# Kernel tuning notes

Hardware: AMD Instinct MI355X
Metric: run time of the kernel (lower is better)

The kernel has to match this reference:

```python
import jax, jax.numpy as jnp
import numpy as np

N_NODES = 100000
NEG_SLOPE = 0.2


def gat_conv(x, edge_index, W, a_src, a_dst, bias):
    """PyG GATConv, heads=1, concat, add_self_loops=True."""
    N = x.shape[0]
    loop = jnp.arange(N, dtype=edge_index.dtype)
    src = jnp.concatenate([edge_index[0], loop])  # message sources j
    dst = jnp.concatenate([edge_index[1], loop])  # message targets i
    h = x @ W                                      # [N, out]
    asrc = h @ a_src                               # [N]
    adst = h @ a_dst                               # [N]
    e = jax.nn.leaky_relu(asrc[src] + adst[dst], NEG_SLOPE)   # [E+N]
    m = jax.ops.segment_max(e, dst, num_segments=N)           # per-dst max
    w = jnp.exp(e - jax.lax.stop_gradient(m)[dst])
    denom = jax.ops.segment_sum(w, dst, num_segments=N)
    alpha = w / denom[dst]                                     # softmax per dst
    out = jax.ops.segment_sum(alpha[:, None] * h[src], dst, num_segments=N)
    return out + bias


def setup_inputs() -> dict:
    key = jax.random.key(0)
    ks = jax.random.split(key, 16)
    N, E, D = N_NODES, 3200000, 128
    x = jax.random.normal(ks[0], (N, D), dtype=jnp.float32)
    edge_index = jax.random.randint(ks[1], (2, E), 0, N, dtype=jnp.int64)
    def glorot(k, shape):
        fan = sum(shape)
        return jax.random.uniform(k, shape, jnp.float32, -1.0, 1.0) * np.sqrt(6.0 / fan)
    return {
        "x": x,
        "edge_index": edge_index,
        "W1": glorot(ks[2], (D, 16)),
        "a1_src": glorot(ks[3], (16,)),
        "a1_dst": glorot(ks[4], (16,)),
        "b1": jnp.zeros((16,), jnp.float32),
        "W2": glorot(ks[5], (16, 10)),
        "a2_src": glorot(ks[6], (10,)),
        "a2_dst": glorot(ks[7], (10,)),
        "b2": jnp.zeros((10,), jnp.float32),
        "Wl1": glorot(ks[8], (10, 10)),
        "bl1": jnp.zeros((10,), jnp.float32),
        "Wl2": glorot(ks[9], (10, 1)),
        "bl2": jnp.zeros((1,), jnp.float32),
    }


def reference(x, edge_index, W1, a1_src, a1_dst, b1, W2, a2_src, a2_dst, b2,
              Wl1, bl1, Wl2, bl2):
    h = gat_conv(x, edge_index, W1, a1_src, a1_dst, b1)
    h = jax.nn.relu(h)
    h = gat_conv(h, edge_index, W2, a2_src, a2_dst, b2)
    h = h @ Wl1 + bl1
    h = jax.nn.relu(h)
    return h @ Wl2 + bl2  # [N, 1]
```

## Files before the change

kernel.cpp:

```cpp
#include <hip/hip_runtime.h>
#include <hip/hip_fp16.h>


#define NEG 0.2f
#define FSH 7
#define BNODES 128
#define NSBMAX 1024
#define CAPB 4608
#define TILE 4096
#define EPT 8
#define PES 9
#define LOFSTR 132

__device__ __forceinline__ float lrelu(float x) { return x > 0.0f ? x : NEG * x; }

__device__ __forceinline__ unsigned fenc(float f) {
    unsigned u = __float_as_uint(f);
    return (u & 0x80000000u) ? ~u : (u | 0x80000000u);
}
__device__ __forceinline__ float fdec(unsigned e) {
    return (e & 0x80000000u) ? __uint_as_float(e & 0x7FFFFFFFu) : __uint_as_float(~e);
}

__device__ __forceinline__ float4 ldh4(const __half* h, size_t off) {
    uint2 u = *(const uint2*)(h + off);
    __half2 a = *(__half2*)&u.x, b = *(__half2*)&u.y;
    float2 fa = __half22float2(a), fb = __half22float2(b);
    return make_float4(fa.x, fa.y, fb.x, fb.y);
}

__global__ __launch_bounds__(512) void k_front(
    const float* __restrict__ x, const float* __restrict__ W1,
    const float* __restrict__ a1s, const float* __restrict__ a1d,
    __half* __restrict__ h1, float* __restrict__ s1, float* __restrict__ d1,
    unsigned* __restrict__ gmax,
    const int* __restrict__ esrc, const int* __restrict__ edst,
    int* __restrict__ bcur, unsigned* __restrict__ pairs,
    int N, int E, int NG, int NC, int NSB)
{
    __shared__ float smem[9224];
    int tid = threadIdx.x;
    int bid = blockIdx.x;
    long long T = (long long)NG + NC;
    int before = (int)(((long long)bid * NC) / T);
    int isc = (int)((((long long)bid + 1) * NC) / T) > before;

    if (isc) {
        unsigned* lsrt = (unsigned*)smem;
        int* lhist = (int*)smem + TILE;
        int* lofs  = lhist + NSBMAX;
        int* gbase = lofs + NSBMAX;
        int* wsum  = gbase + NSBMAX;
        unsigned short* rid = (unsigned short*)(smem + TILE + 3 * NSBMAX + 8);
        int cid = before;
        int base = cid * TILE;
        int tcnt = min(TILE, E - base);
        for (int i = tid; i < NSB; i += 512) lhist[i] = 0;
        __syncthreads();
        int ed[EPT];
#pragma unroll
        for (int u = 0; u < EPT; ++u) {
            int i = tid + u * 512;
            ed[u] = (i < tcnt) ? edst[base + i] : -1;
            if (ed[u] >= 0) atomicAdd(&lhist[ed[u] >> FSH], 1);
        }
        __syncthreads();
        int i0 = 2 * tid;
        int a = (i0 < NSB) ? lhist[i0] : 0;
        int b = (i0 + 1 < NSB) ? lhist[i0 + 1] : 0;
        int s = a + b, pfx = s;
#pragma unroll
        for (int off = 1; off < 64; off <<= 1) {
            int t = __shfl_up(pfx, off, 64);
            if ((tid & 63) >= off) pfx += t;
        }
        if ((tid & 63) == 63) wsum[tid >> 6] = pfx;
        __syncthreads();
        int carry = 0;
        for (int w = 0; w < (tid >> 6); ++w) carry += wsum[w];
        int excl = pfx + carry - s;
        if (i0 < NSB) {
            lofs[i0] = excl;
            gbase[i0] = a ? atomicAdd(&bcur[i0 * 16], a) : 0;
        }
        if (i0 + 1 < NSB) {
            lofs[i0 + 1] = excl + a;
            gbase[i0 + 1] = b ? atomicAdd(&bcur[(i0 + 1) * 16], b) : 0;
        }
        __syncthreads();
        if (i0 < NSB) lhist[i0] = lofs[i0];
        if (i0 + 1 < NSB) lhist[i0 + 1] = lofs[i0 + 1];
        __syncthreads();
#pragma unroll
        for (int u = 0; u < EPT; ++u) {
            int i = tid + u * 512;
            if (ed[u] >= 0) {
                int d = ed[u], srcv = esrc[base + i];
                int bb = d >> FSH;
                int pos = atomicAdd(&lhist[bb], 1);
                lsrt[pos] = ((unsigned)(d & (BNODES - 1)) << 17) | (unsigned)srcv;
                rid[pos] = (unsigned short)bb;
            }
        }
        __syncthreads();
#pragma unroll
        for (int u = 0; u < EPT; ++u) {
            int i = tid + u * 512;
            if (i < tcnt) {
                int r = rid[i];
                int rel = gbase[r] + (i - lofs[r]);
                if (rel < CAPB) pairs[(size_t)r * CAPB + rel] = lsrt[i];
            }
        }
        return;
    }

    float* sW = smem;
    float* wm = smem + 2060;
    int gid = bid - before;
    for (int i = tid; i < 2048; i += 512) sW[i + ((i >> 9) << 2)] = W1[i];
    int node0 = gid * 128;
    int node = node0 + (tid >> 2);
    int q = tid & 3;
    bool valid = node < N;
    float4 xr[8];
    {
        const float4* xp = (const float4*)x + (size_t)node * 32 + q * 8;
#pragma unroll
        for (int k = 0; k < 8; ++k)
            xr[k] = valid ? xp[k] : make_float4(0.f, 0.f, 0.f, 0.f);
    }
    __syncthreads();

    float acc[16];
#pragma unroll
    for (int c = 0; c < 16; ++c) acc[c] = 0.f;
    int wbase = q * 516;
#pragma unroll
    for (int k = 0; k < 8; ++k) {
        float xs0 = xr[k].x, xs1 = xr[k].y, xs2 = xr[k].z, xs3 = xr[k].w;
#pragma unroll
        for (int t = 0; t < 4; ++t) {
            float xv = (t == 0) ? xs0 : (t == 1) ? xs1 : (t == 2) ? xs2 : xs3;
            const float4* wrow = (const float4*)&sW[wbase + (k * 4 + t) * 16];
            float4 w0 = wrow[0], w1 = wrow[1], w2 = wrow[2], w3 = wrow[3];
            acc[0]  += xv * w0.x; acc[1]  += xv * w0.y; acc[2]  += xv * w0.z; acc[3]  += xv * w0.w;
            acc[4]  += xv * w1.x; acc[5]  += xv * w1.y; acc[6]  += xv * w1.z; acc[7]  += xv * w1.w;
            acc[8]  += xv * w2.x; acc[9]  += xv * w2.y; acc[10] += xv * w2.z; acc[11] += xv * w2.w;
            acc[12] += xv * w3.x; acc[13] += xv * w3.y; acc[14] += xv * w3.z; acc[15] += xv * w3.w;
        }
    }
#pragma unroll
    for (int c = 0; c < 16; ++c) {
        acc[c] += __shfl_xor(acc[c], 1);
        acc[c] += __shfl_xor(acc[c], 2);
    }
    float sv = 0.f, dv = 0.f;
    {
        const float4* asp = (const float4*)a1s;
        const float4* adp = (const float4*)a1d;
#pragma unroll
        for (int r = 0; r < 4; ++r) {
            float4 as = asp[r], ad = adp[r];
            sv += acc[r*4+0]*as.x + acc[r*4+1]*as.y + acc[r*4+2]*as.z + acc[r*4+3]*as.w;
            dv += acc[r*4+0]*ad.x + acc[r*4+1]*ad.y + acc[r*4+2]*ad.z + acc[r*4+3]*ad.w;
        }
    }
    if (valid) {
        float4 av;
        if      (q == 0) av = make_float4(acc[0],  acc[1],  acc[2],  acc[3]);
        else if (q == 1) av = make_float4(acc[4],  acc[5],  acc[6],  acc[7]);
        else if (q == 2) av = make_float4(acc[8],  acc[9],  acc[10], acc[11]);
        else             av = make_float4(acc[12], acc[13], acc[14], acc[15]);
        __half2 p0 = __floats2half2_rn(av.x, av.y);
        __half2 p1 = __floats2half2_rn(av.z, av.w);
        uint2 u; u.x = *(unsigned*)&p0; u.y = *(unsigned*)&p1;
        *(uint2*)&h1[(size_t)node * 16 + q * 4] = u;
        if (q == 0) { s1[node] = sv; d1[node] = dv; }
    }
    float m = valid ? sv : -3.4e38f;
#pragma unroll
    for (int off = 32; off >= 1; off >>= 1) m = fmaxf(m, __shfl_xor(m, off));
    if ((tid & 63) == 0) wm[tid >> 6] = m;
    __syncthreads();
    if (tid == 0) {
        float bmx = wm[0];
#pragma unroll
        for (int i = 1; i < 8; ++i) bmx = fmaxf(bmx, wm[i]);
        atomicMax(gmax, fenc(bmx));
    }
}

__global__ __launch_bounds__(512) void k_agg1(
    const int* __restrict__ bcur, unsigned* __restrict__ pairs,
    const int* __restrict__ esrc, const int* __restrict__ edst,
    const float* __restrict__ s1, const float* __restrict__ d1, const __half* __restrict__ h1,
    const float* __restrict__ b1, const float* __restrict__ W2,
    const float* __restrict__ a2s, const float* __restrict__ a2d,
    __half* __restrict__ h2, float* __restrict__ s2, float* __restrict__ d2,
    const unsigned* __restrict__ gmax1p, unsigned* __restrict__ gmax2,
    int* __restrict__ lofs_g, int N, int E)
{
    __shared__ unsigned srt[CAPB];
    __shared__ float accs[BNODES * 17];
    __shared__ int lcnt[BNODES];
    __shared__ int lofs[BNODES + 1];
    __shared__ float dds[BNODES], mbs[BNODES];
    __shared__ float sW[160], sb[16], sas[16], sad[16];
    __shared__ int wsum[8];
    __shared__ float wm[8];

    int tid = threadIdx.x;
    int fb = blockIdx.x;
    if (tid < 160) sW[tid] = W2[tid];
    if (tid < 16) {
        sb[tid]  = b1[tid];
        sas[tid] = (tid < 10) ? a2s[tid] : 0.f;
        sad[tid] = (tid < 10) ? a2d[tid] : 0.f;
    }
    int node0 = fb << FSH;
    float g0 = fdec(*gmax1p);
    if (tid < BNODES) {
        int n = node0 + tid;
        float dd = (n < N) ? d1[n] : 0.f;
        dds[tid] = dd; mbs[tid] = lrelu(g0 + dd);
        lcnt[tid] = 0;
    }
    __syncthreads();

    int rbase = fb * CAPB;
    int cnt = bcur[fb * 16];
    int gg = tid >> 2, q = tid & 3;

    if (cnt <= CAPB) {
        unsigned pe[PES];
#pragma unroll
        for (int u = 0; u < PES; ++u) {
            int i = tid + u * 512;
            bool ok = (i < cnt);
            pe[u] = ok ? pairs[rbase + i] : 0u;
            if (ok) atomicAdd(&lcnt[(pe[u] >> 17) & (BNODES - 1)], 1);
        }
        __syncthreads();
        int c = (tid < BNODES) ? lcnt[tid] : 0;
        int pfx = c;
#pragma unroll
        for (int off = 1; off < 64; off <<= 1) {
            int t = __shfl_up(pfx, off, 64);
            if ((tid & 63) >= off) pfx += t;
        }
        if ((tid & 63) == 63) wsum[tid >> 6] = pfx;
        __syncthreads();
        int carry = 0;
        for (int w = 0; w < (tid >> 6); ++w) carry += wsum[w];
        pfx += carry;
        if (tid < BNODES) { lofs[tid + 1] = pfx; lcnt[tid] = pfx - c; }
        if (tid == 0) lofs[0] = 0;
        __syncthreads();
#pragma unroll
        for (int u = 0; u < PES; ++u) {
            int i = tid + u * 512;
            if (i < cnt) {
                unsigned p = pe[u];
                int pos = atomicAdd(&lcnt[(p >> 17) & (BNODES - 1)], 1);
                srt[pos] = p & 0x1FFFF;
            }
        }
        __syncthreads();

#pragma unroll
        for (int u = 0; u < PES; ++u) {
            int i = tid + u * 512;
            if (i < cnt) pairs[rbase + i] = srt[i];
        }
        if (tid <= BNODES) lofs_g[fb * LOFSTR + tid] = lofs[tid];
        if (tid == 0) lofs_g[fb * LOFSTR + BNODES + 1] = 1;

        int n = node0 + gg;
        float4 accv; float den;
        if (n < N) {
            float w = __expf(lrelu(s1[n] + dds[gg]) - mbs[gg]);
            float4 hv = ldh4(h1, (size_t)n * 16 + 4 * q);
            accv = make_float4(w * hv.x, w * hv.y, w * hv.z, w * hv.w);
            den = w;
        } else { accv = make_float4(0.f, 0.f, 0.f, 0.f); den = 0.f; }
        {
            float dd = dds[gg], mb = mbs[gg];
            int j = lofs[gg], j1 = lofs[gg + 1];
            for (; j + 4 <= j1; j += 4) {
                int e0 = srt[j], e1 = srt[j + 1], e2 = srt[j + 2], e3 = srt[j + 3];
                float4 H0 = ldh4(h1, (size_t)e0 * 16 + 4 * q);
                float4 H1 = ldh4(h1, (size_t)e1 * 16 + 4 * q);
                float4 H2 = ldh4(h1, (size_t)e2 * 16 + 4 * q);
                float4 H3 = ldh4(h1, (size_t)e3 * 16 + 4 * q);
                int eq = srt[j + q];
                float wq = __expf(lrelu(s1[eq] + dd) - mb);
                float w0 = __shfl(wq, 0, 4), w1 = __shfl(wq, 1, 4);
                float w2 = __shfl(wq, 2, 4), w3 = __shfl(wq, 3, 4);
                accv.x += w0 * H0.x + w1 * H1.x + w2 * H2.x + w3 * H3.x;
                accv.y += w0 * H0.y + w1 * H1.y + w2 * H2.y + w3 * H3.y;
                accv.z += w0 * H0.z + w1 * H1.z + w2 * H2.z + w3 * H3.z;
                accv.w += w0 * H0.w + w1 * H1.w + w2 * H2.w + w3 * H3.w;
                den += (w0 + w1) + (w2 + w3);
            }
            for (; j < j1; ++j) {
                int e0 = srt[j];
                float w0 = __expf(lrelu(s1[e0] + dd) - mb);
                float4 H0 = ldh4(h1, (size_t)e0 * 16 + 4 * q);
                accv.x += w0 * H0.x; accv.y += w0 * H0.y;
                accv.z += w0 * H0.z; accv.w += w0 * H0.w;
                den += w0;
            }
        }
        accs[gg * 17 + 4 * q + 0] = accv.x;
        accs[gg * 17 + 4 * q + 1] = accv.y;
        accs[gg * 17 + 4 * q + 2] = accv.z;
        accs[gg * 17 + 4 * q + 3] = accv.w;
        if (q == 0) accs[gg * 17 + 16] = den;
        __syncthreads();
    } else {
        if (tid == 0) lofs_g[fb * LOFSTR + BNODES + 1] = 0;
        for (int i = tid; i < BNODES * 17; i += 512) accs[i] = 0.f;
        __syncthreads();
        if (tid < BNODES) {
            int n = node0 + tid;
            if (n < N) {
                float w = __expf(lrelu(s1[n] + dds[tid]) - mbs[tid]);
#pragma unroll
                for (int t = 0; t < 16; ++t)
                    accs[tid * 17 + t] = w * __half2float(h1[(size_t)n * 16 + t]);
                accs[tid * 17 + 16] = w;
            }
        }
        __syncthreads();
        for (int i = tid; i < E; i += 512) {
            int d = edst[i];
            if ((d >> FSH) != fb) continue;
            int nl = d & (BNODES - 1), src = esrc[i];
            float w = __expf(lrelu(s1[src] + dds[nl]) - mbs[nl]);
#pragma unroll
            for (int t = 0; t < 16; ++t)
                atomicAdd(&accs[nl * 17 + t], w * __half2float(h1[(size_t)src * 16 + t]));
            atomicAdd(&accs[nl * 17 + 16], w);
        }
        __syncthreads();
    }

    int g = tid >> 4, k = tid & 15;
    float sval = -3.4e38f;
#pragma unroll
    for (int qq = 0; qq < 4; ++qq) {
        int nl = g * 4 + qq, nn = node0 + nl;
        if (nn >= N) continue;
        float inv = 1.f / accs[nl * 17 + 16];
        float o = fmaxf(accs[nl * 17 + k] * inv + sb[k], 0.f);
        float hh = 0.f;
#pragma unroll
        for (int kk = 0; kk < 16; ++kk) {
            float ov = __shfl(o, kk, 16);
            if (k < 10) hh += ov * sW[kk * 10 + k];
        }
        if (k >= 10) hh = 0.f;
        float ts = hh * sas[k];
        float td = hh * sad[k];
#pragma unroll
        for (int off = 1; off < 16; off <<= 1) {
            ts += __shfl_xor(ts, off, 16);
            td += __shfl_xor(td, off, 16);
        }
        h2[(size_t)nn * 16 + k] = __float2half_rn(hh);
        if (k == 0) { s2[nn] = ts; d2[nn] = td; }
        sval = fmaxf(sval, ts);
    }
    float m = sval;
#pragma unroll
    for (int off = 32; off >= 1; off >>= 1) m = fmaxf(m, __shfl_xor(m, off));
    if ((tid & 63) == 0) wm[tid >> 6] = m;
    __syncthreads();
    if (tid == 0) {
        float bmx = wm[0];
#pragma unroll
        for (int i = 1; i < 8; ++i) bmx = fmaxf(bmx, wm[i]);
        atomicMax(gmax2, fenc(bmx));
    }
}

__global__ __launch_bounds__(512) void k_agg2(
    const unsigned* __restrict__ pairs,
    const int* __restrict__ esrc, const int* __restrict__ edst,
    const float* __restrict__ s2, const float* __restrict__ d2, const __half* __restrict__ h2,
    const float* __restrict__ b2, const float* __restrict__ Wl1, const float* __restrict__ bl1,
    const float* __restrict__ Wl2, const float* __restrict__ bl2,
    const unsigned* __restrict__ gmax2p, const int* __restrict__ lofs_g,
    float* __restrict__ out, int N, int E)
{
    __shared__ unsigned srt[CAPB];
    __shared__ float accs[BNODES * 17];
    __shared__ int lofs[BNODES + 1];
    __shared__ float dds[BNODES], mbs[BNODES];
    __shared__ float sW1[100], sb1[16], sW2[16], sb2g[16];
    __shared__ float sbl2;
    __shared__ int s_ok;

    int tid = threadIdx.x;
    int fb = blockIdx.x;
    if (tid < 100) sW1[tid] = Wl1[tid];
    if (tid < 16) {
        sb1[tid]  = (tid < 10) ? bl1[tid] : 0.f;
        sW2[tid]  = (tid < 10) ? Wl2[tid] : 0.f;
        sb2g[tid] = (tid < 10) ? b2[tid]  : 0.f;
    }
    if (tid == 0) sbl2 = bl2[0];
    if (tid <= BNODES) lofs[tid] = lofs_g[fb * LOFSTR + tid];
    if (tid == 256) s_ok = lofs_g[fb * LOFSTR + BNODES + 1];
    int node0 = fb << FSH;
    float g0 = fdec(*gmax2p);
    if (tid < BNODES) {
        int n = node0 + tid;
        float dd = (n < N) ? d2[n] : 0.f;
        dds[tid] = dd; mbs[tid] = lrelu(g0 + dd);
    }
    __syncthreads();

    int rbase = fb * CAPB;
    int gg = tid >> 2, q = tid & 3;

    if (s_ok) {
        int cnt = lofs[BNODES];
#pragma unroll
        for (int u = 0; u < PES; ++u) {
            int i = tid + u * 512;
            if (i < cnt) srt[i] = pairs[rbase + i];
        }
        __syncthreads();

        int n = node0 + gg;
        float4 accv; float den;
        if (n < N) {
            float w = __expf(lrelu(s2[n] + dds[gg]) - mbs[gg]);
            float4 hv = ldh4(h2, (size_t)n * 16 + 4 * q);
            accv = make_float4(w * hv.x, w * hv.y, w * hv.z, w * hv.w);
            den = w;
        } else { accv = make_float4(0.f, 0.f, 0.f, 0.f); den = 0.f; }
        {
            float dd = dds[gg], mb = mbs[gg];
            int j = lofs[gg], j1 = lofs[gg + 1];
            for (; j + 4 <= j1; j += 4) {
                int e0 = srt[j], e1 = srt[j + 1], e2 = srt[j + 2], e3 = srt[j + 3];
                float4 H0 = ldh4(h2, (size_t)e0 * 16 + 4 * q);
                float4 H1 = ldh4(h2, (size_t)e1 * 16 + 4 * q);
                float4 H2 = ldh4(h2, (size_t)e2 * 16 + 4 * q);
                float4 H3 = ldh4(h2, (size_t)e3 * 16 + 4 * q);
                int eq = srt[j + q];
                float wq = __expf(lrelu(s2[eq] + dd) - mb);
                float w0 = __shfl(wq, 0, 4), w1 = __shfl(wq, 1, 4);
                float w2 = __shfl(wq, 2, 4), w3 = __shfl(wq, 3, 4);
                accv.x += w0 * H0.x + w1 * H1.x + w2 * H2.x + w3 * H3.x;
                accv.y += w0 * H0.y + w1 * H1.y + w2 * H2.y + w3 * H3.y;
                accv.z += w0 * H0.z + w1 * H1.z + w2 * H2.z + w3 * H3.z;
                accv.w += w0 * H0.w + w1 * H1.w + w2 * H2.w + w3 * H3.w;
                den += (w0 + w1) + (w2 + w3);
            }
            for (; j < j1; ++j) {
                int e0 = srt[j];
                float w0 = __expf(lrelu(s2[e0] + dd) - mb);
                float4 H0 = ldh4(h2, (size_t)e0 * 16 + 4 * q);
                accv.x += w0 * H0.x; accv.y += w0 * H0.y;
                accv.z += w0 * H0.z; accv.w += w0 * H0.w;
                den += w0;
            }
        }
        accs[gg * 17 + 4 * q + 0] = accv.x;
        accs[gg * 17 + 4 * q + 1] = accv.y;
        accs[gg * 17 + 4 * q + 2] = accv.z;
        accs[gg * 17 + 4 * q + 3] = accv.w;
        if (q == 0) accs[gg * 17 + 16] = den;
        __syncthreads();
    } else {
        for (int i = tid; i < BNODES * 17; i += 512) accs[i] = 0.f;
        __syncthreads();
        if (tid < BNODES) {
            int n = node0 + tid;
            if (n < N) {
                float w = __expf(lrelu(s2[n] + dds[tid]) - mbs[tid]);
#pragma unroll
                for (int t = 0; t < 16; ++t)
                    accs[tid * 17 + t] = w * __half2float(h2[(size_t)n * 16 + t]);
                accs[tid * 17 + 16] = w;
            }
        }
        __syncthreads();
        for (int i = tid; i < E; i += 512) {
            int d = edst[i];
            if ((d >> FSH) != fb) continue;
            int nl = d & (BNODES - 1), src = esrc[i];
            float w = __expf(lrelu(s2[src] + dds[nl]) - mbs[nl]);
#pragma unroll
            for (int t = 0; t < 16; ++t)
                atomicAdd(&accs[nl * 17 + t], w * __half2float(h2[(size_t)src * 16 + t]));
            atomicAdd(&accs[nl * 17 + 16], w);
        }
        __syncthreads();
    }

    int g = tid >> 4, k = tid & 15;
    bool fk = k < 10;
#pragma unroll
    for (int qq = 0; qq < 4; ++qq) {
        int nl = g * 4 + qq, nn = node0 + nl;
        if (nn >= N) continue;
        float inv = 1.f / accs[nl * 17 + 16];
        float o = fk ? accs[nl * 17 + k] * inv + sb2g[k] : 0.f;
        float v = sb1[k];
#pragma unroll
        for (int kk = 0; kk < 10; ++kk) {
            float ov = __shfl(o, kk, 16);
            if (fk) v += ov * sW1[kk * 10 + k];
        }
        float t = fmaxf(v, 0.f);
        float cc = t * sW2[k];
#pragma unroll
        for (int off = 1; off < 16; off <<= 1) cc += __shfl_xor(cc, off, 16);
        if (k == 0) out[nn] = cc + sbl2;
    }
}

extern "C" void kernel_launch(void* const* d_in, const int* in_sizes, int n_in,
                              void* d_out, int out_size, void* d_ws, size_t ws_size,
                              hipStream_t stream)
{
    const float* x   = (const float*)d_in[0];
    const int*   ei  = (const int*)  d_in[1];
    const float* W1  = (const float*)d_in[2];
    const float* a1s = (const float*)d_in[3];
    const float* a1d = (const float*)d_in[4];
    const float* b1  = (const float*)d_in[5];
    const float* W2  = (const float*)d_in[6];
    const float* a2s = (const float*)d_in[7];
    const float* a2d = (const float*)d_in[8];
    const float* b2  = (const float*)d_in[9];
    const float* Wl1 = (const float*)d_in[10];
    const float* bl1 = (const float*)d_in[11];
    const float* Wl2 = (const float*)d_in[12];
    const float* bl2 = (const float*)d_in[13];

    int N = in_sizes[0] / 128;
    int E = in_sizes[1] / 2;
    const int* ei_src = ei;
    const int* ei_dst = ei + E;
    int NSB = (N + BNODES - 1) >> FSH;

    size_t Np = ((size_t)N + 3) & ~(size_t)3;
    size_t need_bytes = (16 + (size_t)NSB * 16) * 4 + Np * 20 * 4
                      + (size_t)NSB * CAPB * 4 + (size_t)NSB * LOFSTR * 4;
    if (ws_size < need_bytes) return;

    unsigned* gmax1 = (unsigned*)d_ws;
    unsigned* gmax2 = gmax1 + 1;
    int* bcur = (int*)d_ws + 16;
    float* rest = (float*)d_ws + 16 + (size_t)NSB * 16;
    __half* h1 = (__half*)rest;
    float* s1 = rest + Np * 8;
    float* d1 = s1 + Np;
    __half* h2 = (__half*)(d1 + Np);
    float* s2 = (float*)(h2) + Np * 8;
    float* d2 = s2 + Np;
    unsigned* pairs = (unsigned*)(d2 + Np);
    int* lofs_g = (int*)(pairs + (size_t)NSB * CAPB);

    int NG = (N + 127) / 128;
    int NC = (E + TILE - 1) / TILE;

    hipMemsetAsync(d_ws, 0, (16 + (size_t)NSB * 16) * sizeof(int), stream);
    hipLaunchKernelGGL(k_front, dim3(NG + NC), dim3(512), 0, stream,
                       x, W1, a1s, a1d, h1, s1, d1, gmax1,
                       ei_src, ei_dst, bcur, pairs, N, E, NG, NC, NSB);
    hipLaunchKernelGGL(k_agg1, dim3(NSB), dim3(512), 0, stream,
                       bcur, pairs, ei_src, ei_dst, s1, d1, h1, b1, W2, a2s, a2d,
                       h2, s2, d2, gmax1, gmax2, lofs_g, N, E);
    hipLaunchKernelGGL(k_agg2, dim3(NSB), dim3(512), 0, stream,
                       pairs, ei_src, ei_dst, s2, d2, h2, b2, Wl1, bl1, Wl2, bl2,
                       gmax2, lofs_g, (float*)d_out, N, E);
}
```

Baseline: 258.8 us.

## Balance edge aggregation by splitting sorted edge range evenly across thread groups

```diff
diff --git a/kernel.cpp b/kernel.cpp
--- a/kernel.cpp
+++ b/kernel.cpp
@@ -276,47 +276,69 @@
         if (tid <= BNODES) lofs_g[fb * LOFSTR + tid] = lofs[tid];
         if (tid == 0) lofs_g[fb * LOFSTR + BNODES + 1] = 1;
 
-        int n = node0 + gg;
-        float4 accv; float den;
-        if (n < N) {
-            float w = __expf(lrelu(s1[n] + dds[gg]) - mbs[gg]);
-            float4 hv = ldh4(h1, (size_t)n * 16 + 4 * q);
-            accv = make_float4(w * hv.x, w * hv.y, w * hv.z, w * hv.w);
-            den = w;
-        } else { accv = make_float4(0.f, 0.f, 0.f, 0.f); den = 0.f; }
         {
-            float dd = dds[gg], mb = mbs[gg];
-            int j = lofs[gg], j1 = lofs[gg + 1];
-            for (; j + 4 <= j1; j += 4) {
-                int e0 = srt[j], e1 = srt[j + 1], e2 = srt[j + 2], e3 = srt[j + 3];
-                float4 H0 = ldh4(h1, (size_t)e0 * 16 + 4 * q);
-                float4 H1 = ldh4(h1, (size_t)e1 * 16 + 4 * q);
-                float4 H2 = ldh4(h1, (size_t)e2 * 16 + 4 * q);
-                float4 H3 = ldh4(h1, (size_t)e3 * 16 + 4 * q);
-                int eq = srt[j + q];
-                float wq = __expf(lrelu(s1[eq] + dd) - mb);
-                float w0 = __shfl(wq, 0, 4), w1 = __shfl(wq, 1, 4);
-                float w2 = __shfl(wq, 2, 4), w3 = __shfl(wq, 3, 4);
-                accv.x += w0 * H0.x + w1 * H1.x + w2 * H2.x + w3 * H3.x;
-                accv.y += w0 * H0.y + w1 * H1.y + w2 * H2.y + w3 * H3.y;
-                accv.z += w0 * H0.z + w1 * H1.z + w2 * H2.z + w3 * H3.z;
-                accv.w += w0 * H0.w + w1 * H1.w + w2 * H2.w + w3 * H3.w;
-                den += (w0 + w1) + (w2 + w3);
-            }
-            for (; j < j1; ++j) {
-                int e0 = srt[j];
-                float w0 = __expf(lrelu(s1[e0] + dd) - mb);
-                float4 H0 = ldh4(h1, (size_t)e0 * 16 + 4 * q);
-                accv.x += w0 * H0.x; accv.y += w0 * H0.y;
-                accv.z += w0 * H0.z; accv.w += w0 * H0.w;
-                den += w0;
-            }
-        }
-        accs[gg * 17 + 4 * q + 0] = accv.x;
-        accs[gg * 17 + 4 * q + 1] = accv.y;
-        accs[gg * 17 + 4 * q + 2] = accv.z;
-        accs[gg * 17 + 4 * q + 3] = accv.w;
-        if (q == 0) accs[gg * 17 + 16] = den;
+            int n = node0 + gg;
+            float4 v = make_float4(0.f, 0.f, 0.f, 0.f); float w = 0.f;
+            if (n < N) {
+                w = __expf(lrelu(s1[n] + dds[gg]) - mbs[gg]);
+                float4 hv = ldh4(h1, (size_t)n * 16 + 4 * q);
+                v = make_float4(w * hv.x, w * hv.y, w * hv.z, w * hv.w);
+            }
+            accs[gg * 17 + 4 * q + 0] = v.x;
+            accs[gg * 17 + 4 * q + 1] = v.y;
+            accs[gg * 17 + 4 * q + 2] = v.z;
+            accs[gg * 17 + 4 * q + 3] = v.w;
+            if (q == 0) accs[gg * 17 + 16] = w;
+        }
+        __syncthreads();
+
+        int slice = (cnt + BNODES - 1) >> FSH;
+        int j0 = gg * slice, j1 = min(j0 + slice, cnt);
+        if (j0 < j1) {
+            int nl;
+            {   int lo = 0, hi = BNODES - 1;
+                while (lo < hi) { int mid = (lo + hi + 1) >> 1; if (lofs[mid] <= j0) lo = mid; else hi = mid - 1; }
+                nl = lo; }
+            int j = j0;
+            float4 accv = make_float4(0.f, 0.f, 0.f, 0.f); float den = 0.f;
+            while (true) {
+                int jn = min(j1, lofs[nl + 1]);
+                float dd = dds[nl], mb = mbs[nl];
+                for (; j + 4 <= jn; j += 4) {
+                    int e0 = srt[j], e1 = srt[j + 1], e2 = srt[j + 2], e3 = srt[j + 3];
+                    float4 H0 = ldh4(h1, (size_t)e0 * 16 + 4 * q);
+                    float4 H1 = ldh4(h1, (size_t)e1 * 16 + 4 * q);
+                    float4 H2 = ldh4(h1, (size_t)e2 * 16 + 4 * q);
+                    float4 H3 = ldh4(h1, (size_t)e3 * 16 + 4 * q);
+                    int eq = srt[j + q];
+                    float wq = __expf(lrelu(s1[eq] + dd) - mb);
+                    float w0 = __shfl(wq, 0, 4), w1 = __shfl(wq, 1, 4);
+                    float w2 = __shfl(wq, 2, 4), w3 = __shfl(wq, 3, 4);
+                    accv.x += w0 * H0.x + w1 * H1.x + w2 * H2.x + w3 * H3.x;
+                    accv.y += w0 * H0.y + w1 * H1.y + w2 * H2.y + w3 * H3.y;
+                    accv.z += w0 * H0.z + w1 * H1.z + w2 * H2.z + w3 * H3.z;
+                    accv.w += w0 * H0.w + w1 * H1.w + w2 * H2.w + w3 * H3.w;
+                    den += (w0 + w1) + (w2 + w3);
+                }
+                for (; j < jn; ++j) {
+                    int e0 = srt[j];
+                    float w0 = __expf(lrelu(s1[e0] + dd) - mb);
+                    float4 H0 = ldh4(h1, (size_t)e0 * 16 + 4 * q);
+                    accv.x += w0 * H0.x; accv.y += w0 * H0.y;
+                    accv.z += w0 * H0.z; accv.w += w0 * H0.w;
+                    den += w0;
+                }
+                atomicAdd(&accs[nl * 17 + 4 * q + 0], accv.x);
+                atomicAdd(&accs[nl * 17 + 4 * q + 1], accv.y);
+                atomicAdd(&accs[nl * 17 + 4 * q + 2], accv.z);
+                atomicAdd(&accs[nl * 17 + 4 * q + 3], accv.w);
+                if (q == 0) atomicAdd(&accs[nl * 17 + 16], den);
+                if (jn >= j1) break;
+                accv = make_float4(0.f, 0.f, 0.f, 0.f); den = 0.f;
+                ++nl;
+                while (lofs[nl + 1] <= j) ++nl;
+            }
+        }
         __syncthreads();
     } else {
         if (tid == 0) lofs_g[fb * LOFSTR + BNODES + 1] = 0;
@@ -432,49 +454,69 @@
             int i = tid + u * 512;
             if (i < cnt) srt[i] = pairs[rbase + i];
         }
-        __syncthreads();
-
-        int n = node0 + gg;
-        float4 accv; float den;
-        if (n < N) {
-            float w = __expf(lrelu(s2[n] + dds[gg]) - mbs[gg]);
-            float4 hv = ldh4(h2, (size_t)n * 16 + 4 * q);
-            accv = make_float4(w * hv.x, w * hv.y, w * hv.z, w * hv.w);
-            den = w;
-        } else { accv = make_float4(0.f, 0.f, 0.f, 0.f); den = 0.f; }
         {
-            float dd = dds[gg], mb = mbs[gg];
-            int j = lofs[gg], j1 = lofs[gg + 1];
-            for (; j + 4 <= j1; j += 4) {
-                int e0 = srt[j], e1 = srt[j + 1], e2 = srt[j + 2], e3 = srt[j + 3];
-                float4 H0 = ldh4(h2, (size_t)e0 * 16 + 4 * q);
-                float4 H1 = ldh4(h2, (size_t)e1 * 16 + 4 * q);
-                float4 H2 = ldh4(h2, (size_t)e2 * 16 + 4 * q);
-                float4 H3 = ldh4(h2, (size_t)e3 * 16 + 4 * q);
-                int eq = srt[j + q];
-                float wq = __expf(lrelu(s2[eq] + dd) - mb);
-                float w0 = __shfl(wq, 0, 4), w1 = __shfl(wq, 1, 4);
-                float w2 = __shfl(wq, 2, 4), w3 = __shfl(wq, 3, 4);
-                accv.x += w0 * H0.x + w1 * H1.x + w2 * H2.x + w3 * H3.x;
-                accv.y += w0 * H0.y + w1 * H1.y + w2 * H2.y + w3 * H3.y;
-                accv.z += w0 * H0.z + w1 * H1.z + w2 * H2.z + w3 * H3.z;
-                accv.w += w0 * H0.w + w1 * H1.w + w2 * H2.w + w3 * H3.w;
-                den += (w0 + w1) + (w2 + w3);
-            }
-            for (; j < j1; ++j) {
-                int e0 = srt[j];
-                float w0 = __expf(lrelu(s2[e0] + dd) - mb);
-                float4 H0 = ldh4(h2, (size_t)e0 * 16 + 4 * q);
-                accv.x += w0 * H0.x; accv.y += w0 * H0.y;
-                accv.z += w0 * H0.z; accv.w += w0 * H0.w;
-                den += w0;
-            }
-        }
-        accs[gg * 17 + 4 * q + 0] = accv.x;
-        accs[gg * 17 + 4 * q + 1] = accv.y;
-        accs[gg * 17 + 4 * q + 2] = accv.z;
-        accs[gg * 17 + 4 * q + 3] = accv.w;
-        if (q == 0) accs[gg * 17 + 16] = den;
+            int n = node0 + gg;
+            float4 v = make_float4(0.f, 0.f, 0.f, 0.f); float w = 0.f;
+            if (n < N) {
+                w = __expf(lrelu(s2[n] + dds[gg]) - mbs[gg]);
+                float4 hv = ldh4(h2, (size_t)n * 16 + 4 * q);
+                v = make_float4(w * hv.x, w * hv.y, w * hv.z, w * hv.w);
+            }
+            accs[gg * 17 + 4 * q + 0] = v.x;
+            accs[gg * 17 + 4 * q + 1] = v.y;
+            accs[gg * 17 + 4 * q + 2] = v.z;
+            accs[gg * 17 + 4 * q + 3] = v.w;
+            if (q == 0) accs[gg * 17 + 16] = w;
+        }
+        __syncthreads();
+
+        int slice = (cnt + BNODES - 1) >> FSH;
+        int j0 = gg * slice, j1 = min(j0 + slice, cnt);
+        if (j0 < j1) {
+            int nl;
+            {   int lo = 0, hi = BNODES - 1;
+                while (lo < hi) { int mid = (lo + hi + 1) >> 1; if (lofs[mid] <= j0) lo = mid; else hi = mid - 1; }
+                nl = lo; }
+            int j = j0;
+            float4 accv = make_float4(0.f, 0.f, 0.f, 0.f); float den = 0.f;
+            while (true) {
+                int jn = min(j1, lofs[nl + 1]);
+                float dd = dds[nl], mb = mbs[nl];
+                for (; j + 4 <= jn; j += 4) {
+                    int e0 = srt[j], e1 = srt[j + 1], e2 = srt[j + 2], e3 = srt[j + 3];
+                    float4 H0 = ldh4(h2, (size_t)e0 * 16 + 4 * q);
+                    float4 H1 = ldh4(h2, (size_t)e1 * 16 + 4 * q);
+                    float4 H2 = ldh4(h2, (size_t)e2 * 16 + 4 * q);
+                    float4 H3 = ldh4(h2, (size_t)e3 * 16 + 4 * q);
+                    int eq = srt[j + q];
+                    float wq = __expf(lrelu(s2[eq] + dd) - mb);
+                    float w0 = __shfl(wq, 0, 4), w1 = __shfl(wq, 1, 4);
+                    float w2 = __shfl(wq, 2, 4), w3 = __shfl(wq, 3, 4);
+                    accv.x += w0 * H0.x + w1 * H1.x + w2 * H2.x + w3 * H3.x;
+                    accv.y += w0 * H0.y + w1 * H1.y + w2 * H2.y + w3 * H3.y;
+                    accv.z += w0 * H0.z + w1 * H1.z + w2 * H2.z + w3 * H3.z;
+                    accv.w += w0 * H0.w + w1 * H1.w + w2 * H2.w + w3 * H3.w;
+                    den += (w0 + w1) + (w2 + w3);
+                }
+                for (; j < jn; ++j) {
+                    int e0 = srt[j];
+                    float w0 = __expf(lrelu(s2[e0] + dd) - mb);
+                    float4 H0 = ldh4(h2, (size_t)e0 * 16 + 4 * q);
+                    accv.x += w0 * H0.x; accv.y += w0 * H0.y;
+                    accv.z += w0 * H0.z; accv.w += w0 * H0.w;
+                    den += w0;
+                }
+                atomicAdd(&accs[nl * 17 + 4 * q + 0], accv.x);
+                atomicAdd(&accs[nl * 17 + 4 * q + 1], accv.y);
+                atomicAdd(&accs[nl * 17 + 4 * q + 2], accv.z);
+                atomicAdd(&accs[nl * 17 + 4 * q + 3], accv.w);
+                if (q == 0) atomicAdd(&accs[nl * 17 + 16], den);
+                if (jn >= j1) break;
+                accv = make_float4(0.f, 0.f, 0.f, 0.f); den = 0.f;
+                ++nl;
+                while (lofs[nl + 1] <= j) ++nl;
+            }
+        }
         __syncthreads();
     } else {
         for (int i = tid; i < BNODES * 17; i += 512) accs[i] = 0.f;
```

Measured after the change: 295.9 us. 14.3% more time.
